# Kernel tuning notes

Measured on AMD Instinct MI355X. Metric: run time of the kernel, lower is better.

The kernel has to match this reference:

```python
import math
import jax, jax.numpy as jnp
import numpy as np

# MLA dims (DeepSeek-style, scaled)
B, S, H = 1, 2048, 2048
NH = 16            # num attention heads
DN = 128           # qk_nope_head_dim
DR = 64            # qk_rope_head_dim
DV = 128           # v_head_dim
QL = 1536          # q_lora_rank
KL = 512           # kv_lora_rank
EPS = 1e-6         # rms_norm_eps
ROPE_BASE = 10000.0


def setup_inputs() -> dict:
    key = jax.random.key(0)
    ks = jax.random.split(key, 6)
    w = 0.02  # weight init scale to keep activations sane
    return {
        "hidden": jax.random.normal(ks[0], (B, S, H), jnp.float32),
        "w_kv_a": jax.random.normal(ks[1], (H, QL + KL + DR), jnp.float32) * w,
        "q_a_gamma": jnp.ones((QL,), jnp.float32),
        "w_qb": jax.random.normal(ks[2], (QL, NH * (DN + DR)), jnp.float32) * w,
        "kv_a_gamma": jnp.ones((KL,), jnp.float32),
        "w_kvb": jax.random.normal(ks[3], (KL, NH * (DN + DV)), jnp.float32) * w,
        "w_o": jax.random.normal(ks[4], (NH * DV, H), jnp.float32) * w,
    }


def _rmsnorm(x, gamma, eps=EPS):
    return x * gamma * jax.lax.rsqrt(jnp.mean(x * x, axis=-1, keepdims=True) + eps)


def _rope_tables(seq_len, dim, dtype):
    inv_freq = 1.0 / (ROPE_BASE ** (jnp.arange(0, dim, 2, dtype=jnp.float32) / dim))
    ang = jnp.arange(seq_len, dtype=jnp.float32)[:, None] * inv_freq  # [S, dim/2]
    cos = jnp.concatenate([jnp.cos(ang)] * 2, axis=-1).astype(dtype)  # [S, dim]
    sin = jnp.concatenate([jnp.sin(ang)] * 2, axis=-1).astype(dtype)
    return cos[None, :, None, :], sin[None, :, None, :]  # broadcast to [B,S,h,dim]


def _rotate_half(x):
    h = x.shape[-1] // 2
    return jnp.concatenate([-x[..., h:], x[..., :h]], axis=-1)


def reference(hidden, w_kv_a, q_a_gamma, w_qb, kv_a_gamma, w_kvb, w_o):
    b, s, _ = hidden.shape
    # Fused down-projection: [compressed_q | compressed_kv | k_rope]
    fused = hidden @ w_kv_a                          # [B,S,QL+KL+DR]
    q_c = fused[..., :QL]
    kv_c = fused[..., QL:QL + KL]
    k_pe = fused[..., QL + KL:]                      # [B,S,DR], shared across heads (MQA rope)

    # Q up-projection from normalized latent
    q = _rmsnorm(q_c, q_a_gamma) @ w_qb              # [B,S,NH*(DN+DR)]
    q = q.reshape(b, s, NH, DN + DR)
    q_nope, q_pe = q[..., :DN], q[..., DN:]

    # KV up-projection from normalized latent
    kv = _rmsnorm(kv_c, kv_a_gamma) @ w_kvb          # [B,S,NH*(DN+DV)]
    kv = kv.reshape(b, s, NH, DN + DV)
    k_nope, v = kv[..., :DN], kv[..., DN:]

    # RoPE on the rope slices only
    cos, sin = _rope_tables(s, DR, hidden.dtype)
    q_pe = q_pe * cos + _rotate_half(q_pe) * sin     # [B,S,NH,DR]
    k_pe = k_pe[:, :, None, :]
    k_pe = k_pe * cos + _rotate_half(k_pe) * sin     # [B,S,1,DR]

    q_full = jnp.concatenate([q_nope, q_pe], axis=-1)                         # [B,S,NH,DN+DR]
    k_full = jnp.concatenate([k_nope, jnp.broadcast_to(k_pe, (b, s, NH, DR))], axis=-1)

    scale = 1.0 / math.sqrt(DN + DR)
    scores = jnp.einsum('bqhd,bkhd->bhqk', q_full, k_full) * scale            # [B,NH,S,S]
    pos = jnp.arange(s)
    causal = pos[:, None] >= pos[None, :]
    scores = jnp.where(causal[None, None], scores, jnp.asarray(-1e30, scores.dtype))
    probs = jax.nn.softmax(scores, axis=-1)
    attn = jnp.einsum('bhqk,bkhd->bqhd', probs, v)                            # [B,S,NH,DV]
    return attn.reshape(b, s, NH * DV) @ w_o                                  # [B,S,H]
```

## Files before the change

### kernel.cpp

```cpp
#include <hip/hip_runtime.h>
#include <math.h>

#define S_LEN 2048
#define NH 16
#define DN 128
#define DR 64
#define DV 128
#define QL 1536
#define KL 512
#define FUSED_N 2112
#define FPAD 2176
#define QB_N 3072
#define KVB_N 4096
#define HD_QK 192
#define EPS_RMS 1e-6f

typedef _Float16 f16;
typedef _Float16 half8 __attribute__((ext_vector_type(8)));
typedef _Float16 half4 __attribute__((ext_vector_type(4)));
typedef float floatx4 __attribute__((ext_vector_type(4)));

__global__ __launch_bounds__(256) void cvt_f16_k(const float* __restrict__ in,
                                                 f16* __restrict__ out, int n4)
{
    int i = blockIdx.x * 256 + threadIdx.x;
    if (i < n4) {
        float4 v = ((const float4*)in)[i];
        half4 h;
        h[0] = (f16)v.x; h[1] = (f16)v.y; h[2] = (f16)v.z; h[3] = (f16)v.w;
        ((half4*)out)[i] = h;
    }
}

__global__ __launch_bounds__(256) void tconv_k(const float* __restrict__ in,
                                               f16* __restrict__ out,
                                               int K, int N)
{
    __shared__ float t[32][33];
    const int k0 = blockIdx.y * 32, n0 = blockIdx.x * 32;
    const int c = threadIdx.x & 31, r8 = threadIdx.x >> 5;
    #pragma unroll
    for (int i = 0; i < 4; ++i) {
        int r = r8 + i * 8;
        int gc = n0 + c;
        t[r][c] = (gc < N) ? in[(size_t)(k0 + r) * N + gc] : 0.f;
    }
    __syncthreads();
    #pragma unroll
    for (int i = 0; i < 4; ++i) {
        int r = r8 + i * 8;
        out[(size_t)(n0 + r) * K + k0 + c] = (f16)t[c][r];
    }
}

__device__ __forceinline__ void async16(const f16* gp, f16* lp)
{
    __builtin_amdgcn_global_load_lds(
        (const __attribute__((address_space(1))) void*)gp,
        (__attribute__((address_space(3))) void*)lp, 16, 0, 0);
}

template <int OUT_F16>
__global__ __launch_bounds__(256) void gemm_mfma(
    const f16* __restrict__ A,
    const f16* __restrict__ Bt,
    void* __restrict__ Cv, int M, int N, int K)
{
    __shared__ f16 sm[2][2][128 * 64];

    const int tid = threadIdx.x;
    const int wv = tid >> 6, lane = tid & 63;
    const int quad = lane >> 4, l15 = lane & 15;
    const int wr = wv >> 1, wc = wv & 1;
    const int bm = blockIdx.y * 128, bn = blockIdx.x * 128;
    const int srow = lane >> 3;
    const int sc = lane & 7;

    size_t aoff[4], boff[4];
    int ldst[4];
    #pragma unroll
    for (int t = 0; t < 4; ++t) {
        int rl = wv * 32 + t * 8 + srow;
        int ch = sc ^ (rl & 7);
        aoff[t] = (size_t)(bm + rl) * K + ch * 8;
        boff[t] = (size_t)(bn + rl) * K + ch * 8;
        ldst[t] = (wv * 32 + t * 8) * 64;
    }

    #pragma unroll
    for (int t = 0; t < 4; ++t) {
        async16(A  + aoff[t], &sm[0][0][ldst[t]]);
        async16(Bt + boff[t], &sm[0][1][ldst[t]]);
    }

    floatx4 acc[4][4] = {};
    const int nsteps = K >> 6;

    for (int step = 0; step < nsteps; ++step) {
        const int cur = step & 1;
        __syncthreads();
        if (step + 1 < nsteps) {
            const int k0n = (step + 1) << 6;
            f16* Ab = sm[1 - cur][0];
            f16* Bb = sm[1 - cur][1];
            #pragma unroll
            for (int t = 0; t < 4; ++t) {
                async16(A  + aoff[t] + k0n, Ab + ldst[t]);
                async16(Bt + boff[t] + k0n, Bb + ldst[t]);
            }
        }
        const f16* As = sm[cur][0];
        const f16* Bs = sm[cur][1];

        #pragma unroll
        for (int ks = 0; ks < 2; ++ks) {
            half8 av[4], bv[4];
            #pragma unroll
            for (int i = 0; i < 4; ++i) {
                int m = wr * 64 + i * 16 + l15;
                av[i] = *(const half8*)&As[m * 64 + ((ks * 4 + quad) ^ (m & 7)) * 8];
            }
            #pragma unroll
            for (int j = 0; j < 4; ++j) {
                int n = wc * 64 + j * 16 + l15;
                bv[j] = *(const half8*)&Bs[n * 64 + ((ks * 4 + quad) ^ (n & 7)) * 8];
            }
            #pragma unroll
            for (int i = 0; i < 4; ++i)
                #pragma unroll
                for (int j = 0; j < 4; ++j)
                    acc[i][j] = __builtin_amdgcn_mfma_f32_16x16x32_f16(
                        av[i], bv[j], acc[i][j], 0, 0, 0);
        }
    }

    #pragma unroll
    for (int i = 0; i < 4; ++i) {
        int rbase = bm + wr * 64 + i * 16 + quad * 4;
        #pragma unroll
        for (int j = 0; j < 4; ++j) {
            int cidx = bn + wc * 64 + j * 16 + l15;
            #pragma unroll
            for (int rr = 0; rr < 4; ++rr) {
                if (OUT_F16)
                    ((f16*)Cv)[(size_t)(rbase + rr) * N + cidx] = (f16)acc[i][j][rr];
                else
                    ((float*)Cv)[(size_t)(rbase + rr) * N + cidx] = acc[i][j][rr];
            }
        }
    }
}

__global__ __launch_bounds__(256) void rmsnorm_k(
    const float* __restrict__ in, int stride, int ncols,
    const float* __restrict__ gamma, f16* __restrict__ out)
{
    const int row = blockIdx.x;
    const float* x = in + (size_t)row * stride;

    float ss = 0.f;
    for (int c = threadIdx.x; c < ncols; c += 256) {
        float v = x[c];
        ss += v * v;
    }
    #pragma unroll
    for (int off = 32; off > 0; off >>= 1) ss += __shfl_down(ss, off);

    __shared__ float warp_s[4];
    __shared__ float scale_s;
    const int wid = threadIdx.x >> 6;
    if ((threadIdx.x & 63) == 0) warp_s[wid] = ss;
    __syncthreads();
    if (threadIdx.x == 0) {
        float t = warp_s[0] + warp_s[1] + warp_s[2] + warp_s[3];
        scale_s = rsqrtf(t / (float)ncols + EPS_RMS);
    }
    __syncthreads();
    const float sc = scale_s;
    for (int c = threadIdx.x; c < ncols; c += 256)
        out[(size_t)row * ncols + c] = (f16)(x[c] * gamma[c] * sc);
}

__device__ __forceinline__ float rope_one(int s, int d, float x, float other)
{
    const int j = d & 31;
    const float invf = expf(-0.28782313662425572f * (float)j);
    const float ang = (float)s * invf;
    float sn, cs;
    sincosf(ang, &sn, &cs);
    float rot = (d < 32) ? -other : other;
    return x * cs + rot * sn;
}

__global__ __launch_bounds__(256) void rope_q_k(f16* __restrict__ q)
{
    const int s = blockIdx.x;
    const int h = blockIdx.y * 4 + (threadIdx.x >> 6);
    const int d = threadIdx.x & 63;
    f16* base = q + (size_t)s * QB_N + h * HD_QK + DN;
    float x = (float)base[d];
    float other = (float)((d < 32) ? base[d + 32] : base[d - 32]);
    base[d] = (f16)rope_one(s, d, x, other);
}

__global__ __launch_bounds__(256) void kfull_k(const f16* __restrict__ kv,
                                               const float* __restrict__ fused,
                                               f16* __restrict__ kfull)
{
    int n = blockIdx.x * 256 + threadIdx.x;
    int c8 = n % 24;
    int s = (n / 24) & 2047;
    int h = n / (24 * 2048);
    half8 v;
    if (c8 < 16) {
        v = *(const half8*)&kv[(size_t)s * KVB_N + h * 256 + c8 * 8];
    } else {
        const float* src = fused + (size_t)s * FPAD + (QL + KL);
        int dbase = (c8 - 16) * 8;
        #pragma unroll
        for (int j = 0; j < 8; ++j) {
            int d = dbase + j;
            float x = src[d];
            float other = src[(d < 32) ? d + 32 : d - 32];
            v[j] = (f16)rope_one(s, d, x, other);
        }
    }
    *(half8*)&kfull[((size_t)h * S_LEN + s) * HD_QK + c8 * 8] = v;
}

__global__ __launch_bounds__(256) void vt_k(const f16* __restrict__ kv,
                                            f16* __restrict__ vt)
{
    __shared__ f16 t[32][33];
    const int s0 = blockIdx.x * 32, d0 = blockIdx.y * 32, h = blockIdx.z;
    const int tid = threadIdx.x;
    {
        const int c = tid & 31, rb = tid >> 5;
        #pragma unroll
        for (int i = 0; i < 4; ++i) {
            int r = rb + i * 8;
            t[r][c] = kv[(size_t)(s0 + r) * KVB_N + h * 256 + 128 + d0 + c];
        }
    }
    __syncthreads();
    {
        const int d = tid >> 3, s4 = tid & 7;
        half4 v;
        v[0] = t[s4 * 4 + 0][d];
        v[1] = t[s4 * 4 + 1][d];
        v[2] = t[s4 * 4 + 2][d];
        v[3] = t[s4 * 4 + 3][d];
        *(half4*)&vt[((size_t)h * DV + d0 + d) * S_LEN + s0 + s4 * 4] = v;
    }
}

__global__ __launch_bounds__(256) void attn_mfma_k(
    const f16* __restrict__ q,
    const f16* __restrict__ kfull,
    const f16* __restrict__ vt,
    f16* __restrict__ part_o,
    float* __restrict__ part_ml)
{
    __shared__ f16 sm[25088];

    const int tid = threadIdx.x;
    const int w = tid >> 6, lane = tid & 63;
    const int quad = lane >> 4, l15 = lane & 15;
    const int wbase = w * 64;
    const int h = blockIdx.y;
    const int z = blockIdx.z;
    const int qb = (blockIdx.y < 8) ? (int)blockIdx.x : 31 - (int)blockIdx.x;
    const int q0 = qb * 64;
    const int kt_begin = z ? (qb + 1) : 0;
    const int kt_end   = z ? (2 * qb + 2) : (qb + 1);
    const float scale2 = 0.10411755f;

    const f16* kf_h = kfull + (size_t)h * S_LEN * HD_QK;
    const f16* vt_h = vt + (size_t)h * DV * S_LEN;

    int koff[3];
    #pragma unroll
    for (int j = 0; j < 3; ++j) {
        int sig = j * 256 + tid;
        int r = sig / 24, cs = sig - r * 24;
        int ch = (cs & 24) | ((cs & 7) ^ (r & 7));
        koff[j] = r * HD_QK + ch * 8;
    }
    int voff[2];
    #pragma unroll
    for (int j = 0; j < 2; ++j) {
        int sig = j * 256 + tid;
        int rv = sig >> 2, c = (sig & 3) ^ ((rv >> 1) & 3);
        voff[j] = rv * S_LEN + c * 8;
    }

    #pragma unroll
    for (int j = 0; j < 6; ++j) {
        int sig = j * 256 + tid;
        int r = sig / 24, cs = sig - r * 24;
        int ch = (cs & 24) | ((cs & 7) ^ (r & 7));
        async16(q + (size_t)(q0 + r) * QB_N + h * HD_QK + ch * 8,
                sm + 10240 + (j * 256 + wbase) * 8);
    }
    {
        const f16* kg = kf_h + (size_t)kt_begin * 32 * HD_QK;
        const f16* vg = vt_h + kt_begin * 32;
        #pragma unroll
        for (int j = 0; j < 3; ++j) async16(kg + koff[j], sm + (j * 256 + wbase) * 8);
        #pragma unroll
        for (int j = 0; j < 2; ++j) async16(vg + voff[j], sm + 6144 + (j * 256 + wbase) * 8);
    }
    __syncthreads();

    half8 qf[6];
    const int qrow = w * 16 + l15;
    #pragma unroll
    for (int kd = 0; kd < 6; ++kd) {
        int c = kd * 4 + quad;
        int cs = (c & 24) | ((c & 7) ^ (qrow & 7));
        qf[kd] = *(const half8*)&sm[10240 + (qrow * 24 + cs) * 8];
    }

    half8 ones_h;
    #pragma unroll
    for (int j = 0; j < 8; ++j) ones_h[j] = (f16)1.0f;

    floatx4 o[8] = {};
    floatx4 o_l = {};
    float m_i[4];
    #pragma unroll
    for (int r = 0; r < 4; ++r) m_i[r] = -1e30f;

    const int qrow_min = q0 + w * 16;
    f16* Pw = sm + 22528 + w * 640;

    for (int kt = kt_begin; kt < kt_end; ++kt) {
        const int cur = (kt - kt_begin) & 1;
        __syncthreads();
        if (kt + 1 < kt_end) {
            const int nxt = 1 - cur;
            const int k0n = (kt + 1) * 32;
            f16* kb = sm + (nxt ? 10240 : 0);
            f16* vb = sm + (nxt ? 16384 : 6144);
            const f16* kg = kf_h + (size_t)k0n * HD_QK;
            const f16* vg = vt_h + k0n;
            #pragma unroll
            for (int j = 0; j < 3; ++j) async16(kg + koff[j], kb + (j * 256 + wbase) * 8);
            #pragma unroll
            for (int j = 0; j < 2; ++j) async16(vg + voff[j], vb + (j * 256 + wbase) * 8);
        }
        const int k0 = kt * 32;
        if (k0 > qrow_min + 15) continue;

        const f16* kb = sm + (cur ? 10240 : 0);
        const f16* vb = sm + (cur ? 16384 : 6144);

        floatx4 s0 = {}, s1 = {};
        #pragma unroll
        for (int kd = 0; kd < 6; ++kd) {
            int c = kd * 4 + quad;
            int cs = (c & 24) | ((c & 7) ^ (l15 & 7));
            half8 b0 = *(const half8*)&kb[(l15 * 24 + cs) * 8];
            half8 b1 = *(const half8*)&kb[((l15 + 16) * 24 + cs) * 8];
            s0 = __builtin_amdgcn_mfma_f32_16x16x32_f16(qf[kd], b0, s0, 0, 0, 0);
            s1 = __builtin_amdgcn_mfma_f32_16x16x32_f16(qf[kd], b1, s1, 0, 0, 0);
        }

        const bool nm = (k0 + 31 > qrow_min);
        float mt[4];
        #pragma unroll
        for (int r = 0; r < 4; ++r) {
            float v0 = s0[r] * scale2, v1 = s1[r] * scale2;
            if (nm) {
                int row = qrow_min + quad * 4 + r;
                if (k0 + l15 > row)      v0 = -1e30f;
                if (k0 + 16 + l15 > row) v1 = -1e30f;
            }
            s0[r] = v0; s1[r] = v1;
            mt[r] = fmaxf(v0, v1);
        }
        #pragma unroll
        for (int r = 0; r < 4; ++r) {
            mt[r] = fmaxf(mt[r], __shfl_xor(mt[r], 1));
            mt[r] = fmaxf(mt[r], __shfl_xor(mt[r], 2));
            mt[r] = fmaxf(mt[r], __shfl_xor(mt[r], 4));
            mt[r] = fmaxf(mt[r], __shfl_xor(mt[r], 8));
        }
        float alpha[4];
        #pragma unroll
        for (int r = 0; r < 4; ++r) {
            float mn = fmaxf(m_i[r], mt[r]);
            alpha[r] = __builtin_exp2f(m_i[r] - mn);
            m_i[r] = mn;
            s0[r] = __builtin_exp2f(s0[r] - mn);
            s1[r] = __builtin_exp2f(s1[r] - mn);
        }

        #pragma unroll
        for (int r = 0; r < 4; ++r) {
            Pw[(quad * 4 + r) * 40 + l15]      = (f16)s0[r];
            Pw[(quad * 4 + r) * 40 + 16 + l15] = (f16)s1[r];
        }

        #pragma unroll
        for (int nb = 0; nb < 8; ++nb)
            #pragma unroll
            for (int r = 0; r < 4; ++r) o[nb][r] *= alpha[r];
        #pragma unroll
        for (int r = 0; r < 4; ++r) o_l[r] *= alpha[r];

        half8 pa = *(const half8*)&Pw[l15 * 40 + quad * 8];
        o_l = __builtin_amdgcn_mfma_f32_16x16x32_f16(pa, ones_h, o_l, 0, 0, 0);
        #pragma unroll
        for (int nb = 0; nb < 8; ++nb) {
            int rv = nb * 16 + l15;
            int sig = rv * 4 + (quad ^ ((l15 >> 1) & 3));
            half8 vv = *(const half8*)&vb[sig * 8];
            o[nb] = __builtin_amdgcn_mfma_f32_16x16x32_f16(pa, vv, o[nb], 0, 0, 0);
        }
    }

    float inv[4];
    #pragma unroll
    for (int r = 0; r < 4; ++r) inv[r] = (o_l[r] > 0.f) ? 1.f / o_l[r] : 0.f;

    f16* po = part_o + (size_t)z * S_LEN * 2048;
    #pragma unroll
    for (int nb = 0; nb < 8; ++nb) {
        #pragma unroll
        for (int r = 0; r < 4; ++r) {
            int row = q0 + w * 16 + quad * 4 + r;
            po[(size_t)row * (NH * DV) + h * DV + nb * 16 + l15] =
                (f16)(o[nb][r] * inv[r]);
        }
    }
    if (l15 == 0) {
        #pragma unroll
        for (int r = 0; r < 4; ++r) {
            int row = q0 + w * 16 + quad * 4 + r;
            float* ml = part_ml + (((size_t)z * NH + h) * S_LEN + row) * 2;
            ml[0] = m_i[r];
            ml[1] = o_l[r];
        }
    }
}

__global__ __launch_bounds__(256) void attn_comb_k(
    const f16* __restrict__ part_o, const float* __restrict__ part_ml,
    f16* __restrict__ attnb)
{
    int g = blockIdx.x * 256 + threadIdx.x;
    int h = (g >> 4) & 15;
    int s = g >> 8;
    const float* ml0 = part_ml + ((size_t)h * S_LEN + s) * 2;
    const float* ml1 = part_ml + (((size_t)NH + h) * S_LEN + s) * 2;
    float m0 = ml0[0], l0 = ml0[1];
    float m1 = ml1[0], l1 = ml1[1];
    float M = fmaxf(m0, m1);
    float w0 = l0 * __builtin_exp2f(m0 - M);
    float w1 = l1 * __builtin_exp2f(m1 - M);
    float inv = 1.f / (w0 + w1);
    w0 *= inv; w1 *= inv;
    half8 p0 = *(const half8*)&part_o[(size_t)g * 8];
    half8 p1 = *(const half8*)&part_o[(size_t)(524288 + g) * 8];
    half8 r;
    #pragma unroll
    for (int j = 0; j < 8; ++j)
        r[j] = (f16)(w0 * (float)p0[j] + w1 * (float)p1[j]);
    *(half8*)&attnb[(size_t)g * 8] = r;
}

extern "C" void kernel_launch(void* const* d_in, const int* in_sizes, int n_in,
                              void* d_out, int out_size, void* d_ws, size_t ws_size,
                              hipStream_t stream)
{
    const float* hidden   = (const float*)d_in[0];
    const float* w_kv_a   = (const float*)d_in[1];
    const float* q_gamma  = (const float*)d_in[2];
    const float* w_qb     = (const float*)d_in[3];
    const float* kv_gamma = (const float*)d_in[4];
    const float* w_kvb    = (const float*)d_in[5];
    const float* w_o      = (const float*)d_in[6];
    float* out = (float*)d_out;

    char* p = (char*)d_ws;
    f16* hid_h   = (f16*)p;  p += (size_t)2048 * 2048 * 2;
    f16* wkva_t  = (f16*)p;  p += (size_t)2176 * 2048 * 2;
    f16* wqb_t   = (f16*)p;  p += (size_t)3072 * 1536 * 2;
    f16* wkvb_t  = (f16*)p;  p += (size_t)4096 * 512 * 2;
    f16* wo_t    = (f16*)p;  p += (size_t)2048 * 2048 * 2;
    float* fused = (float*)p; p += (size_t)2048 * FPAD * 4;
    f16* q_n     = (f16*)p;  p += (size_t)2048 * QL * 2;
    f16* qbuf    = (f16*)p;  p += (size_t)2048 * QB_N * 2;
    f16* kv_n    = (f16*)p;  p += (size_t)2048 * KL * 2;
    f16* kvbuf   = (f16*)p;  p += (size_t)2048 * KVB_N * 2;
    f16* attnb   = (f16*)p;  p += (size_t)2048 * 2048 * 2;
    f16* part_o  = (f16*)p;  p += (size_t)2 * 2048 * 2048 * 2;
    float* part_ml = (float*)p; p += (size_t)2 * NH * 2048 * 2 * 4;

    f16* kfull = hid_h;
    f16* vt    = (f16*)fused;

    dim3 blk(256);

    cvt_f16_k<<<(2048 * 2048 / 4 + 255) / 256, blk, 0, stream>>>(hidden, hid_h, 2048 * 2048 / 4);
    tconv_k<<<dim3(2176 / 32, 2048 / 32), blk, 0, stream>>>(w_kv_a, wkva_t, 2048, FUSED_N);
    tconv_k<<<dim3(3072 / 32, 1536 / 32), blk, 0, stream>>>(w_qb,   wqb_t,  1536, QB_N);
    tconv_k<<<dim3(4096 / 32,  512 / 32), blk, 0, stream>>>(w_kvb,  wkvb_t,  512, KVB_N);
    tconv_k<<<dim3(2048 / 32, 2048 / 32), blk, 0, stream>>>(w_o,    wo_t,   2048, 2048);

    gemm_mfma<0><<<dim3(FPAD / 128, 2048 / 128), blk, 0, stream>>>(
        hid_h, wkva_t, fused, 2048, FPAD, 2048);

    rmsnorm_k<<<2048, blk, 0, stream>>>(fused, FPAD, QL, q_gamma, q_n);
    rmsnorm_k<<<2048, blk, 0, stream>>>(fused + QL, FPAD, KL, kv_gamma, kv_n);

    gemm_mfma<1><<<dim3(QB_N / 128, 2048 / 128), blk, 0, stream>>>(
        q_n, wqb_t, qbuf, 2048, QB_N, QL);
    gemm_mfma<1><<<dim3(KVB_N / 128, 2048 / 128), blk, 0, stream>>>(
        kv_n, wkvb_t, kvbuf, 2048, KVB_N, KL);

    rope_q_k<<<dim3(2048, 4), blk, 0, stream>>>(qbuf);

    kfull_k<<<16 * 2048 * 24 / 256, blk, 0, stream>>>(kvbuf, fused, kfull);
    vt_k<<<dim3(2048 / 32, 128 / 32, NH), blk, 0, stream>>>(kvbuf, vt);

    attn_mfma_k<<<dim3(32, NH, 2), blk, 0, stream>>>(qbuf, kfull, vt, part_o, part_ml);
    attn_comb_k<<<2048, blk, 0, stream>>>(part_o, part_ml, attnb);

    gemm_mfma<0><<<dim3(2048 / 128, 2048 / 128), blk, 0, stream>>>(
        attnb, wo_t, out, 2048, 2048, 2048);
}
```

Measured before the change: 356.6 us.

## Merge prep, norm, up-projection and post kernels; shrink GEMM tile to 128x64

Several kernel launches become single launches that dispatch on block index: weight conversion and transposes, the two rmsnorms, the Q and KV up-projection GEMMs, and the rope/kfull/vt post-processing. The GEMM tile narrows from 128x128 to 128x64, which doubles the block count for better CU occupancy at the cost of less operand reuse per block. vt moves to its own workspace region so it no longer aliases fused, which the post kernel reads in the same launch. The aim is to cut launch overhead and tail idling between small kernels.

```diff
diff --git a/kernel.cpp b/kernel.cpp
--- a/kernel.cpp
+++ b/kernel.cpp
@@ -20,39 +20,6 @@
 typedef _Float16 half4 __attribute__((ext_vector_type(4)));
 typedef float floatx4 __attribute__((ext_vector_type(4)));
 
-__global__ __launch_bounds__(256) void cvt_f16_k(const float* __restrict__ in,
-                                                 f16* __restrict__ out, int n4)
-{
-    int i = blockIdx.x * 256 + threadIdx.x;
-    if (i < n4) {
-        float4 v = ((const float4*)in)[i];
-        half4 h;
-        h[0] = (f16)v.x; h[1] = (f16)v.y; h[2] = (f16)v.z; h[3] = (f16)v.w;
-        ((half4*)out)[i] = h;
-    }
-}
-
-__global__ __launch_bounds__(256) void tconv_k(const float* __restrict__ in,
-                                               f16* __restrict__ out,
-                                               int K, int N)
-{
-    __shared__ float t[32][33];
-    const int k0 = blockIdx.y * 32, n0 = blockIdx.x * 32;
-    const int c = threadIdx.x & 31, r8 = threadIdx.x >> 5;
-    #pragma unroll
-    for (int i = 0; i < 4; ++i) {
-        int r = r8 + i * 8;
-        int gc = n0 + c;
-        t[r][c] = (gc < N) ? in[(size_t)(k0 + r) * N + gc] : 0.f;
-    }
-    __syncthreads();
-    #pragma unroll
-    for (int i = 0; i < 4; ++i) {
-        int r = r8 + i * 8;
-        out[(size_t)(n0 + r) * K + k0 + c] = (f16)t[c][r];
-    }
-}
-
 __device__ __forceinline__ void async16(const f16* gp, f16* lp)
 {
     __builtin_amdgcn_global_load_lds(
@@ -61,39 +28,39 @@
 }
 
 template <int OUT_F16>
-__global__ __launch_bounds__(256) void gemm_mfma(
-    const f16* __restrict__ A,
-    const f16* __restrict__ Bt,
-    void* __restrict__ Cv, int M, int N, int K)
-{
-    __shared__ f16 sm[2][2][128 * 64];
-
+__device__ __forceinline__ void gemm_core(
+    const f16* __restrict__ A, const f16* __restrict__ Bt,
+    void* __restrict__ Cv, int N, int K, int bm, int bn, f16* sm)
+{
     const int tid = threadIdx.x;
     const int wv = tid >> 6, lane = tid & 63;
     const int quad = lane >> 4, l15 = lane & 15;
     const int wr = wv >> 1, wc = wv & 1;
-    const int bm = blockIdx.y * 128, bn = blockIdx.x * 128;
-    const int srow = lane >> 3;
-    const int sc = lane & 7;
-
-    size_t aoff[4], boff[4];
-    int ldst[4];
+    const int srow = lane >> 3, sc = lane & 7;
+
+    size_t aoff[4]; int lda[4];
     #pragma unroll
     for (int t = 0; t < 4; ++t) {
         int rl = wv * 32 + t * 8 + srow;
         int ch = sc ^ (rl & 7);
         aoff[t] = (size_t)(bm + rl) * K + ch * 8;
+        lda[t] = (wv * 32 + t * 8) * 64;
+    }
+    size_t boff[2]; int ldb[2];
+    #pragma unroll
+    for (int t = 0; t < 2; ++t) {
+        int rl = wv * 16 + t * 8 + srow;
+        int ch = sc ^ (rl & 7);
         boff[t] = (size_t)(bn + rl) * K + ch * 8;
-        ldst[t] = (wv * 32 + t * 8) * 64;
-    }
-
-    #pragma unroll
-    for (int t = 0; t < 4; ++t) {
-        async16(A  + aoff[t], &sm[0][0][ldst[t]]);
-        async16(Bt + boff[t], &sm[0][1][ldst[t]]);
-    }
-
-    floatx4 acc[4][4] = {};
+        ldb[t] = 8192 + (wv * 16 + t * 8) * 64;
+    }
+
+    #pragma unroll
+    for (int t = 0; t < 4; ++t) async16(A  + aoff[t], &sm[lda[t]]);
+    #pragma unroll
+    for (int t = 0; t < 2; ++t) async16(Bt + boff[t], &sm[ldb[t]]);
+
+    floatx4 acc[4][2] = {};
     const int nsteps = K >> 6;
 
     for (int step = 0; step < nsteps; ++step) {
@@ -101,34 +68,32 @@
         __syncthreads();
         if (step + 1 < nsteps) {
             const int k0n = (step + 1) << 6;
-            f16* Ab = sm[1 - cur][0];
-            f16* Bb = sm[1 - cur][1];
-            #pragma unroll
-            for (int t = 0; t < 4; ++t) {
-                async16(A  + aoff[t] + k0n, Ab + ldst[t]);
-                async16(Bt + boff[t] + k0n, Bb + ldst[t]);
-            }
-        }
-        const f16* As = sm[cur][0];
-        const f16* Bs = sm[cur][1];
+            f16* nb = sm + (1 - cur) * 12288;
+            #pragma unroll
+            for (int t = 0; t < 4; ++t) async16(A  + aoff[t] + k0n, nb + lda[t]);
+            #pragma unroll
+            for (int t = 0; t < 2; ++t) async16(Bt + boff[t] + k0n, nb + ldb[t]);
+        }
+        const f16* As = sm + cur * 12288;
+        const f16* Bs = As + 8192;
 
         #pragma unroll
         for (int ks = 0; ks < 2; ++ks) {
-            half8 av[4], bv[4];
+            half8 av[4], bv[2];
             #pragma unroll
             for (int i = 0; i < 4; ++i) {
                 int m = wr * 64 + i * 16 + l15;
                 av[i] = *(const half8*)&As[m * 64 + ((ks * 4 + quad) ^ (m & 7)) * 8];
             }
             #pragma unroll
-            for (int j = 0; j < 4; ++j) {
-                int n = wc * 64 + j * 16 + l15;
+            for (int j = 0; j < 2; ++j) {
+                int n = wc * 32 + j * 16 + l15;
                 bv[j] = *(const half8*)&Bs[n * 64 + ((ks * 4 + quad) ^ (n & 7)) * 8];
             }
             #pragma unroll
             for (int i = 0; i < 4; ++i)
                 #pragma unroll
-                for (int j = 0; j < 4; ++j)
+                for (int j = 0; j < 2; ++j)
                     acc[i][j] = __builtin_amdgcn_mfma_f32_16x16x32_f16(
                         av[i], bv[j], acc[i][j], 0, 0, 0);
         }
@@ -138,8 +103,8 @@
     for (int i = 0; i < 4; ++i) {
         int rbase = bm + wr * 64 + i * 16 + quad * 4;
         #pragma unroll
-        for (int j = 0; j < 4; ++j) {
-            int cidx = bn + wc * 64 + j * 16 + l15;
+        for (int j = 0; j < 2; ++j) {
+            int cidx = bn + wc * 32 + j * 16 + l15;
             #pragma unroll
             for (int rr = 0; rr < 4; ++rr) {
                 if (OUT_F16)
@@ -151,12 +116,88 @@
     }
 }
 
+template <int OUT_F16>
+__global__ __launch_bounds__(256) void gemm_mfma(
+    const f16* __restrict__ A, const f16* __restrict__ Bt,
+    void* __restrict__ Cv, int N, int K)
+{
+    __shared__ f16 sm[2 * 12288];
+    gemm_core<OUT_F16>(A, Bt, Cv, N, K, blockIdx.y * 128, blockIdx.x * 64, sm);
+}
+
+__global__ __launch_bounds__(256) void gemm_dual(
+    const f16* __restrict__ A1, const f16* __restrict__ B1, f16* __restrict__ C1,
+    const f16* __restrict__ A2, const f16* __restrict__ B2, f16* __restrict__ C2)
+{
+    __shared__ f16 sm[2 * 12288];
+    int bx = blockIdx.x;
+    if (bx < 48)
+        gemm_core<1>(A1, B1, C1, QB_N, QL, blockIdx.y * 128, bx * 64, sm);
+    else
+        gemm_core<1>(A2, B2, C2, KVB_N, KL, blockIdx.y * 128, (bx - 48) * 64, sm);
+}
+
+__device__ __forceinline__ void tconv_core(
+    const float* __restrict__ in, f16* __restrict__ out,
+    int K, int N, int n0, int k0, float t[32][33])
+{
+    const int c = threadIdx.x & 31, r8 = threadIdx.x >> 5;
+    #pragma unroll
+    for (int i = 0; i < 4; ++i) {
+        int r = r8 + i * 8;
+        int gc = n0 + c;
+        t[r][c] = (gc < N) ? in[(size_t)(k0 + r) * N + gc] : 0.f;
+    }
+    __syncthreads();
+    #pragma unroll
+    for (int i = 0; i < 4; ++i) {
+        int r = r8 + i * 8;
+        out[(size_t)(n0 + r) * K + k0 + c] = (f16)t[c][r];
+    }
+}
+
+__global__ __launch_bounds__(256) void prep_k(
+    const float* __restrict__ hidden, f16* __restrict__ hid_h,
+    const float* __restrict__ w_kv_a, f16* __restrict__ wkva_t,
+    const float* __restrict__ w_qb,   f16* __restrict__ wqb_t,
+    const float* __restrict__ w_kvb,  f16* __restrict__ wkvb_t,
+    const float* __restrict__ w_o,    f16* __restrict__ wo_t)
+{
+    __shared__ float t[32][33];
+    int b = blockIdx.x;
+    if (b < 4096) {
+        int i = b * 256 + threadIdx.x;
+        float4 v = ((const float4*)hidden)[i];
+        half4 h;
+        h[0] = (f16)v.x; h[1] = (f16)v.y; h[2] = (f16)v.z; h[3] = (f16)v.w;
+        ((half4*)hid_h)[i] = h;
+    } else if (b < 8448) {
+        int r = b - 4096;
+        tconv_core(w_kv_a, wkva_t, 2048, FUSED_N, (r % 68) * 32, (r / 68) * 32, t);
+    } else if (b < 13056) {
+        int r = b - 8448;
+        tconv_core(w_qb, wqb_t, QL, QB_N, (r % 96) * 32, (r / 96) * 32, t);
+    } else if (b < 15104) {
+        int r = b - 13056;
+        tconv_core(w_kvb, wkvb_t, KL, KVB_N, (r % 128) * 32, (r / 128) * 32, t);
+    } else {
+        int r = b - 15104;
+        tconv_core(w_o, wo_t, 2048, 2048, (r % 64) * 32, (r / 64) * 32, t);
+    }
+}
+
 __global__ __launch_bounds__(256) void rmsnorm_k(
-    const float* __restrict__ in, int stride, int ncols,
-    const float* __restrict__ gamma, f16* __restrict__ out)
-{
-    const int row = blockIdx.x;
-    const float* x = in + (size_t)row * stride;
+    const float* __restrict__ fused, const float* __restrict__ q_gamma,
+    const float* __restrict__ kv_gamma, f16* __restrict__ q_n,
+    f16* __restrict__ kv_n)
+{
+    const int b = blockIdx.x;
+    const bool isq = b < 2048;
+    const int row = isq ? b : b - 2048;
+    const int ncols = isq ? QL : KL;
+    const float* x = fused + (size_t)row * FPAD + (isq ? 0 : QL);
+    const float* gamma = isq ? q_gamma : kv_gamma;
+    f16* out = isq ? q_n : kv_n;
 
     float ss = 0.f;
     for (int c = threadIdx.x; c < ncols; c += 256) {
@@ -172,8 +213,8 @@
     if ((threadIdx.x & 63) == 0) warp_s[wid] = ss;
     __syncthreads();
     if (threadIdx.x == 0) {
-        float t = warp_s[0] + warp_s[1] + warp_s[2] + warp_s[3];
-        scale_s = rsqrtf(t / (float)ncols + EPS_RMS);
+        float tt = warp_s[0] + warp_s[1] + warp_s[2] + warp_s[3];
+        scale_s = rsqrtf(tt / (float)ncols + EPS_RMS);
     }
     __syncthreads();
     const float sc = scale_s;
@@ -192,65 +233,63 @@
     return x * cs + rot * sn;
 }
 
-__global__ __launch_bounds__(256) void rope_q_k(f16* __restrict__ q)
-{
-    const int s = blockIdx.x;
-    const int h = blockIdx.y * 4 + (threadIdx.x >> 6);
-    const int d = threadIdx.x & 63;
-    f16* base = q + (size_t)s * QB_N + h * HD_QK + DN;
-    float x = (float)base[d];
-    float other = (float)((d < 32) ? base[d + 32] : base[d - 32]);
-    base[d] = (f16)rope_one(s, d, x, other);
-}
-
-__global__ __launch_bounds__(256) void kfull_k(const f16* __restrict__ kv,
-                                               const float* __restrict__ fused,
-                                               f16* __restrict__ kfull)
-{
-    int n = blockIdx.x * 256 + threadIdx.x;
-    int c8 = n % 24;
-    int s = (n / 24) & 2047;
-    int h = n / (24 * 2048);
-    half8 v;
-    if (c8 < 16) {
-        v = *(const half8*)&kv[(size_t)s * KVB_N + h * 256 + c8 * 8];
+__global__ __launch_bounds__(256) void post_k(
+    f16* __restrict__ q, const f16* __restrict__ kv,
+    const float* __restrict__ fused, f16* __restrict__ kfull,
+    f16* __restrict__ vt)
+{
+    __shared__ f16 t[32][33];
+    int b = blockIdx.x;
+    if (b < 8192) {
+        const int s = b & 2047;
+        const int h = (b >> 11) * 4 + (threadIdx.x >> 6);
+        const int d = threadIdx.x & 63;
+        f16* base = q + (size_t)s * QB_N + h * HD_QK + DN;
+        float x = (float)base[d];
+        float other = (float)((d < 32) ? base[d + 32] : base[d - 32]);
+        base[d] = (f16)rope_one(s, d, x, other);
+    } else if (b < 11264) {
+        int n = (b - 8192) * 256 + threadIdx.x;
+        int c8 = n % 24;
+        int s = (n / 24) & 2047;
+        int h = n / (24 * 2048);
+        half8 v;
+        if (c8 < 16) {
+            v = *(const half8*)&kv[(size_t)s * KVB_N + h * 256 + c8 * 8];
+        } else {
+            const float* src = fused + (size_t)s * FPAD + (QL + KL);
+            int dbase = (c8 - 16) * 8;
+            #pragma unroll
+            for (int j = 0; j < 8; ++j) {
+                int d = dbase + j;
+                float x = src[d];
+                float other = src[(d < 32) ? d + 32 : d - 32];
+                v[j] = (f16)rope_one(s, d, x, other);
+            }
+        }
+        *(half8*)&kfull[((size_t)h * S_LEN + s) * HD_QK + c8 * 8] = v;
     } else {
-        const float* src = fused + (size_t)s * FPAD + (QL + KL);
-        int dbase = (c8 - 16) * 8;
-        #pragma unroll
-        for (int j = 0; j < 8; ++j) {
-            int d = dbase + j;
-            float x = src[d];
-            float other = src[(d < 32) ? d + 32 : d - 32];
-            v[j] = (f16)rope_one(s, d, x, other);
-        }
-    }
-    *(half8*)&kfull[((size_t)h * S_LEN + s) * HD_QK + c8 * 8] = v;
-}
-
-__global__ __launch_bounds__(256) void vt_k(const f16* __restrict__ kv,
-                                            f16* __restrict__ vt)
-{
-    __shared__ f16 t[32][33];
-    const int s0 = blockIdx.x * 32, d0 = blockIdx.y * 32, h = blockIdx.z;
-    const int tid = threadIdx.x;
-    {
-        const int c = tid & 31, rb = tid >> 5;
-        #pragma unroll
-        for (int i = 0; i < 4; ++i) {
-            int r = rb + i * 8;
-            t[r][c] = kv[(size_t)(s0 + r) * KVB_N + h * 256 + 128 + d0 + c];
-        }
-    }
-    __syncthreads();
-    {
-        const int d = tid >> 3, s4 = tid & 7;
-        half4 v;
-        v[0] = t[s4 * 4 + 0][d];
-        v[1] = t[s4 * 4 + 1][d];
-        v[2] = t[s4 * 4 + 2][d];
-        v[3] = t[s4 * 4 + 3][d];
-        *(half4*)&vt[((size_t)h * DV + d0 + d) * S_LEN + s0 + s4 * 4] = v;
+        int r = b - 11264;
+        const int s0 = (r & 63) * 32, d0 = ((r >> 6) & 3) * 32, h = r >> 8;
+        const int tid = threadIdx.x;
+        {
+            const int c = tid & 31, rb = tid >> 5;
+            #pragma unroll
+            for (int i = 0; i < 4; ++i) {
+                int rr = rb + i * 8;
+                t[rr][c] = kv[(size_t)(s0 + rr) * KVB_N + h * 256 + 128 + d0 + c];
+            }
+        }
+        __syncthreads();
+        {
+            const int d = tid >> 3, s4 = tid & 7;
+            half4 v;
+            v[0] = t[s4 * 4 + 0][d];
+            v[1] = t[s4 * 4 + 1][d];
+            v[2] = t[s4 * 4 + 2][d];
+            v[3] = t[s4 * 4 + 3][d];
+            *(half4*)&vt[((size_t)h * DV + d0 + d) * S_LEN + s0 + s4 * 4] = v;
+        }
     }
 }
 
@@ -499,35 +538,26 @@
     float* part_ml = (float*)p; p += (size_t)2 * NH * 2048 * 2 * 4;
 
     f16* kfull = hid_h;
-    f16* vt    = (f16*)fused;
+    f16* vt    = (f16*)p;
 
     dim3 blk(256);
 
-    cvt_f16_k<<<(2048 * 2048 / 4 + 255) / 256, blk, 0, stream>>>(hidden, hid_h, 2048 * 2048 / 4);
-    tconv_k<<<dim3(2176 / 32, 2048 / 32), blk, 0, stream>>>(w_kv_a, wkva_t, 2048, FUSED_N);
-    tconv_k<<<dim3(3072 / 32, 1536 / 32), blk, 0, stream>>>(w_qb,   wqb_t,  1536, QB_N);
-    tconv_k<<<dim3(4096 / 32,  512 / 32), blk, 0, stream>>>(w_kvb,  wkvb_t,  512, KVB_N);
-    tconv_k<<<dim3(2048 / 32, 2048 / 32), blk, 0, stream>>>(w_o,    wo_t,   2048, 2048);
-
-    gemm_mfma<0><<<dim3(FPAD / 128, 2048 / 128), blk, 0, stream>>>(
-        hid_h, wkva_t, fused, 2048, FPAD, 2048);
-
-    rmsnorm_k<<<2048, blk, 0, stream>>>(fused, FPAD, QL, q_gamma, q_n);
-    rmsnorm_k<<<2048, blk, 0, stream>>>(fused + QL, FPAD, KL, kv_gamma, kv_n);
-
-    gemm_mfma<1><<<dim3(QB_N / 128, 2048 / 128), blk, 0, stream>>>(
-        q_n, wqb_t, qbuf, 2048, QB_N, QL);
-    gemm_mfma<1><<<dim3(KVB_N / 128, 2048 / 128), blk, 0, stream>>>(
-        kv_n, wkvb_t, kvbuf, 2048, KVB_N, KL);
-
-    rope_q_k<<<dim3(2048, 4), blk, 0, stream>>>(qbuf);
-
-    kfull_k<<<16 * 2048 * 24 / 256, blk, 0, stream>>>(kvbuf, fused, kfull);
-    vt_k<<<dim3(2048 / 32, 128 / 32, NH), blk, 0, stream>>>(kvbuf, vt);
+    prep_k<<<19200, blk, 0, stream>>>(hidden, hid_h, w_kv_a, wkva_t,
+                                      w_qb, wqb_t, w_kvb, wkvb_t, w_o, wo_t);
+
+    gemm_mfma<0><<<dim3(FPAD / 64, 16), blk, 0, stream>>>(
+        hid_h, wkva_t, fused, FPAD, 2048);
+
+    rmsnorm_k<<<4096, blk, 0, stream>>>(fused, q_gamma, kv_gamma, q_n, kv_n);
+
+    gemm_dual<<<dim3(48 + 64, 16), blk, 0, stream>>>(
+        q_n, wqb_t, qbuf, kv_n, wkvb_t, kvbuf);
+
+    post_k<<<15360, blk, 0, stream>>>(qbuf, kvbuf, fused, kfull, vt);
 
     attn_mfma_k<<<dim3(32, NH, 2), blk, 0, stream>>>(qbuf, kfull, vt, part_o, part_ml);
     attn_comb_k<<<2048, blk, 0, stream>>>(part_o, part_ml, attnb);
 
-    gemm_mfma<0><<<dim3(2048 / 128, 2048 / 128), blk, 0, stream>>>(
-        attnb, wo_t, out, 2048, 2048, 2048);
-}
+    gemm_mfma<0><<<dim3(2048 / 64, 16), blk, 0, stream>>>(
+        attnb, wo_t, out, 2048, 2048);
+}
```

New measurement: 328.4 us. 1.09x faster.
